# Kernel optimization log

Hardware: AMD Instinct MI355X
Metric: run time of the kernel (lower is better)

Reference implementation:

```python
import jax, jax.numpy as jnp
import numpy as np

# Haar step along H (axis 1 of a (B,H,W) image): average / abs-diff of row pairs.
def _haar_y(img):
    odd, even = img[:, 0::2], img[:, 1::2]
    return (odd + even) / 2.0, jnp.abs(odd - even)

# Haar step along W (axis 2). In the original torch code this is done via
# permute + flip + Y-transform + permute + flip-back; the two flips act on the
# untouched H axis and cancel exactly, so the math reduces to pairing along W.
def _haar_x(img):
    odd, even = img[:, :, 0::2], img[:, :, 1::2]
    return (odd + even) / 2.0, jnp.abs(odd - even)

def _dwt2(img):  # (B,H,W) -> LL, LH, HL, HH each (B,H/2,W/2)
    L, H = _haar_y(img)
    LL, LH = _haar_x(L)
    HL, HH = _haar_x(H)
    return LL, LH, HL, HH

def setup_inputs() -> dict:
    key = jax.random.key(0)
    x = jax.random.uniform(key, (32, 3, 512, 512), dtype=jnp.float32)
    return {"x": x}

def reference(x):
    r, g, b = x[:, 0], x[:, 1], x[:, 2]
    # Level 1
    r1 = _dwt2(r); g1 = _dwt2(g); b1 = _dwt2(b)
    t1 = jnp.stack([*r1, *g1, *b1], axis=1)  # (B,12,H/2,W/2)
    # Level 2 (recursion on LL of each channel)
    r2 = _dwt2(r1[0]); g2 = _dwt2(g1[0]); b2 = _dwt2(b1[0])
    t2 = jnp.stack([*r2, *g2, *b2], axis=1)
    # Level 3
    r3 = _dwt2(r2[0]); g3 = _dwt2(g2[0]); b3 = _dwt2(b2[0])
    t3 = jnp.stack([*r3, *g3, *b3], axis=1)
    # Level 4 -- faithfully reproduces the original bug: the blue-channel
    # level-4 bands are computed from wavelet_L4/H4 left over from the green
    # channel, so b4 == g4.
    r4 = _dwt2(r3[0]); g4 = _dwt2(g3[0]); b4 = g4
    t4 = jnp.stack([*r4, *g4, *b4], axis=1)
    return (t1, t2, t3, t4)
```

## Files before the change

### kernel.cpp

```cpp
#include <hip/hip_runtime.h>

__global__ __launch_bounds__(256) void dwt_level_kernel(
    const float* __restrict__ src, float* __restrict__ dst,
    int W,
    int h, int shift,
    long src_b_stride, long src_c_stride,
    int nC, int dup)
{
    int pid = blockIdx.x * blockDim.x + threadIdx.x;
    int npix = h << shift;
    if (pid >= npix) return;

    int plane = blockIdx.y;
    int b = plane / nC;
    int c = plane - b * nC;

    int jw = pid & ((1 << shift) - 1);
    int i  = pid >> shift;

    const float* sp = src + (long)b * src_b_stride + (long)c * src_c_stride;
    const float4 r0 = *((const float4*)(sp + (long)(2 * i)     * W) + jw);
    const float4 r1 = *((const float4*)(sp + (long)(2 * i + 1) * W) + jw);

    float L00 = (r0.x + r1.x) * 0.5f;
    float L01 = (r0.y + r1.y) * 0.5f;
    float H00 = fabsf(r0.x - r1.x);
    float H01 = fabsf(r0.y - r1.y);
    float L10 = (r0.z + r1.z) * 0.5f;
    float L11 = (r0.w + r1.w) * 0.5f;
    float H10 = fabsf(r0.z - r1.z);
    float H11 = fabsf(r0.w - r1.w);

    float2 ll = make_float2((L00 + L01) * 0.5f, (L10 + L11) * 0.5f);
    float2 lh = make_float2(fabsf(L00 - L01), fabsf(L10 - L11));
    float2 hl = make_float2((H00 + H01) * 0.5f, (H10 + H11) * 0.5f);
    float2 hh = make_float2(fabsf(H00 - H01), fabsf(H10 - H11));

    int w = 2 << shift;
    long hw = (long)h * w;
    float* dp = dst + (long)(b * 12 + 4 * c) * hw + (long)i * w + 2 * jw;

    *(float2*)(dp + 0 * hw) = ll;
    *(float2*)(dp + 1 * hw) = lh;
    *(float2*)(dp + 2 * hw) = hl;
    *(float2*)(dp + 3 * hw) = hh;

    if (dup && c == nC - 1) {
        float* dp2 = dp + 4 * hw;
        *(float2*)(dp2 + 0 * hw) = ll;
        *(float2*)(dp2 + 1 * hw) = lh;
        *(float2*)(dp2 + 2 * hw) = hl;
        *(float2*)(dp2 + 3 * hw) = hh;
    }
}

extern "C" void kernel_launch(void* const* d_in, const int* in_sizes, int n_in,
                              void* d_out, int out_size, void* d_ws, size_t ws_size,
                              hipStream_t stream) {
    const float* x = (const float*)d_in[0];
    float* out = (float*)d_out;

    const long t1_off = 0;
    const long t2_off = t1_off + 32L * 12 * 256 * 256;
    const long t3_off = t2_off + 32L * 12 * 128 * 128;
    const long t4_off = t3_off + 32L * 12 * 64 * 64;

    dim3 blk(256);
    dwt_level_kernel<<<dim3(128, 96), blk, 0, stream>>>(
        x, out + t1_off, 512, 256, 7, 3L * 512 * 512, 512L * 512, 3, 0);
    dwt_level_kernel<<<dim3(32, 96), blk, 0, stream>>>(
        out + t1_off, out + t2_off, 256, 128, 6, 12L * 256 * 256, 4L * 256 * 256, 3, 0);
    dwt_level_kernel<<<dim3(8, 96), blk, 0, stream>>>(
        out + t2_off, out + t3_off, 128, 64, 5, 12L * 128 * 128, 4L * 128 * 128, 3, 0);
    dwt_level_kernel<<<dim3(2, 64), blk, 0, stream>>>(
        out + t3_off, out + t4_off, 64, 32, 4, 12L * 64 * 64, 4L * 64 * 64, 2, 1);
}
```

Measured before the change: 215.7 us.

## Fuse all four Haar DWT levels into one tiled kernel using LDS

Replaces four per-level launches with a single kernel where each block owns a 64x64 input tile per channel plane. It computes level 1 from global memory and keeps each level's LL band in shared memory to compute levels 2-4. This removes the global re-reads of intermediate LL bands and three kernel launches. The cost is more idle threads at the deeper levels, extra block barriers, and narrow per-row stores for the smaller levels.

Result: slower. 223.0 us (+3.4%).

```diff
diff --git a/kernel.cpp b/kernel.cpp
--- a/kernel.cpp
+++ b/kernel.cpp
@@ -1,56 +1,125 @@
 #include <hip/hip_runtime.h>
 
-__global__ __launch_bounds__(256) void dwt_level_kernel(
-    const float* __restrict__ src, float* __restrict__ dst,
-    int W,
-    int h, int shift,
-    long src_b_stride, long src_c_stride,
-    int nC, int dup)
+__global__ __launch_bounds__(256) void dwt_fused_kernel(
+    const float* __restrict__ x, float* __restrict__ out)
 {
-    int pid = blockIdx.x * blockDim.x + threadIdx.x;
-    int npix = h << shift;
-    if (pid >= npix) return;
+    __shared__ float lds1[32 * 36];
+    __shared__ float lds2[16 * 18];
+    __shared__ float lds3[8 * 9];
 
-    int plane = blockIdx.y;
-    int b = plane / nC;
-    int c = plane - b * nC;
+    const int t = threadIdx.x;
+    const int tile = blockIdx.x;
+    const int tx = tile & 7, ty = tile >> 3;
+    const int plane = blockIdx.y;
+    const int b = plane / 3, c = plane - 3 * b;
 
-    int jw = pid & ((1 << shift) - 1);
-    int i  = pid >> shift;
+    const long pbase = (long)(b * 12 + c * 4);
+    const long off2 = 25165824L;
+    const long off3 = 31457280L;
+    const long off4 = 33030144L;
 
-    const float* sp = src + (long)b * src_b_stride + (long)c * src_c_stride;
-    const float4 r0 = *((const float4*)(sp + (long)(2 * i)     * W) + jw);
-    const float4 r1 = *((const float4*)(sp + (long)(2 * i + 1) * W) + jw);
+    {
+        const int oi = t >> 3;
+        const int oj = t & 7;
+        const float* sp = x + (long)(b * 3 + c) * (512 * 512);
+        const int gr = ty * 64 + 2 * oi;
+        const int gc = tx * 64 + 8 * oj;
+        const float4 r0a = *(const float4*)(sp + (long)gr * 512 + gc);
+        const float4 r0b = *(const float4*)(sp + (long)gr * 512 + gc + 4);
+        const float4 r1a = *(const float4*)(sp + (long)(gr + 1) * 512 + gc);
+        const float4 r1b = *(const float4*)(sp + (long)(gr + 1) * 512 + gc + 4);
 
-    float L00 = (r0.x + r1.x) * 0.5f;
-    float L01 = (r0.y + r1.y) * 0.5f;
-    float H00 = fabsf(r0.x - r1.x);
-    float H01 = fabsf(r0.y - r1.y);
-    float L10 = (r0.z + r1.z) * 0.5f;
-    float L11 = (r0.w + r1.w) * 0.5f;
-    float H10 = fabsf(r0.z - r1.z);
-    float H11 = fabsf(r0.w - r1.w);
+        float L0 = (r0a.x + r1a.x) * 0.5f, L1 = (r0a.y + r1a.y) * 0.5f;
+        float H0 = fabsf(r0a.x - r1a.x),   H1 = fabsf(r0a.y - r1a.y);
+        float L2 = (r0a.z + r1a.z) * 0.5f, L3 = (r0a.w + r1a.w) * 0.5f;
+        float H2 = fabsf(r0a.z - r1a.z),   H3 = fabsf(r0a.w - r1a.w);
+        float L4 = (r0b.x + r1b.x) * 0.5f, L5 = (r0b.y + r1b.y) * 0.5f;
+        float H4 = fabsf(r0b.x - r1b.x),   H5 = fabsf(r0b.y - r1b.y);
+        float L6 = (r0b.z + r1b.z) * 0.5f, L7 = (r0b.w + r1b.w) * 0.5f;
+        float H6 = fabsf(r0b.z - r1b.z),   H7 = fabsf(r0b.w - r1b.w);
 
-    float2 ll = make_float2((L00 + L01) * 0.5f, (L10 + L11) * 0.5f);
-    float2 lh = make_float2(fabsf(L00 - L01), fabsf(L10 - L11));
-    float2 hl = make_float2((H00 + H01) * 0.5f, (H10 + H11) * 0.5f);
-    float2 hh = make_float2(fabsf(H00 - H01), fabsf(H10 - H11));
+        float4 ll = make_float4((L0 + L1) * 0.5f, (L2 + L3) * 0.5f,
+                                (L4 + L5) * 0.5f, (L6 + L7) * 0.5f);
+        float4 lh = make_float4(fabsf(L0 - L1), fabsf(L2 - L3),
+                                fabsf(L4 - L5), fabsf(L6 - L7));
+        float4 hl = make_float4((H0 + H1) * 0.5f, (H2 + H3) * 0.5f,
+                                (H4 + H5) * 0.5f, (H6 + H7) * 0.5f);
+        float4 hh = make_float4(fabsf(H0 - H1), fabsf(H2 - H3),
+                                fabsf(H4 - H5), fabsf(H6 - H7));
 
-    int w = 2 << shift;
-    long hw = (long)h * w;
-    float* dp = dst + (long)(b * 12 + 4 * c) * hw + (long)i * w + 2 * jw;
+        float* dp = out + (long)(ty * 32 + oi) * 256 + (tx * 32 + 4 * oj);
+        *(float4*)(dp + (pbase + 0) * 65536) = ll;
+        *(float4*)(dp + (pbase + 1) * 65536) = lh;
+        *(float4*)(dp + (pbase + 2) * 65536) = hl;
+        *(float4*)(dp + (pbase + 3) * 65536) = hh;
 
-    *(float2*)(dp + 0 * hw) = ll;
-    *(float2*)(dp + 1 * hw) = lh;
-    *(float2*)(dp + 2 * hw) = hl;
-    *(float2*)(dp + 3 * hw) = hh;
+        *(float4*)(lds1 + oi * 36 + 4 * oj) = ll;
+    }
+    __syncthreads();
 
-    if (dup && c == nC - 1) {
-        float* dp2 = dp + 4 * hw;
-        *(float2*)(dp2 + 0 * hw) = ll;
-        *(float2*)(dp2 + 1 * hw) = lh;
-        *(float2*)(dp2 + 2 * hw) = hl;
-        *(float2*)(dp2 + 3 * hw) = hh;
+    {
+        const int i2 = t >> 4, j2 = t & 15;
+        float a  = lds1[(2 * i2) * 36 + 2 * j2];
+        float bb = lds1[(2 * i2) * 36 + 2 * j2 + 1];
+        float cc = lds1[(2 * i2 + 1) * 36 + 2 * j2];
+        float dd = lds1[(2 * i2 + 1) * 36 + 2 * j2 + 1];
+        float L0 = (a + cc) * 0.5f, L1 = (bb + dd) * 0.5f;
+        float Ha = fabsf(a - cc),   Hb = fabsf(bb - dd);
+        float ll = (L0 + L1) * 0.5f, lh = fabsf(L0 - L1);
+        float hl = (Ha + Hb) * 0.5f, hh = fabsf(Ha - Hb);
+
+        float* dp = out + off2 + (long)(ty * 16 + i2) * 128 + (tx * 16 + j2);
+        dp[(pbase + 0) * 16384] = ll;
+        dp[(pbase + 1) * 16384] = lh;
+        dp[(pbase + 2) * 16384] = hl;
+        dp[(pbase + 3) * 16384] = hh;
+        lds2[i2 * 18 + j2] = ll;
+    }
+    __syncthreads();
+
+    if (t < 64) {
+        const int i3 = t >> 3, j3 = t & 7;
+        float a  = lds2[(2 * i3) * 18 + 2 * j3];
+        float bb = lds2[(2 * i3) * 18 + 2 * j3 + 1];
+        float cc = lds2[(2 * i3 + 1) * 18 + 2 * j3];
+        float dd = lds2[(2 * i3 + 1) * 18 + 2 * j3 + 1];
+        float L0 = (a + cc) * 0.5f, L1 = (bb + dd) * 0.5f;
+        float Ha = fabsf(a - cc),   Hb = fabsf(bb - dd);
+        float ll = (L0 + L1) * 0.5f, lh = fabsf(L0 - L1);
+        float hl = (Ha + Hb) * 0.5f, hh = fabsf(Ha - Hb);
+
+        float* dp = out + off3 + (long)(ty * 8 + i3) * 64 + (tx * 8 + j3);
+        dp[(pbase + 0) * 4096] = ll;
+        dp[(pbase + 1) * 4096] = lh;
+        dp[(pbase + 2) * 4096] = hl;
+        dp[(pbase + 3) * 4096] = hh;
+        lds3[i3 * 9 + j3] = ll;
+    }
+    __syncthreads();
+
+    if (t < 16 && c < 2) {
+        const int i4 = t >> 2, j4 = t & 3;
+        float a  = lds3[(2 * i4) * 9 + 2 * j4];
+        float bb = lds3[(2 * i4) * 9 + 2 * j4 + 1];
+        float cc = lds3[(2 * i4 + 1) * 9 + 2 * j4];
+        float dd = lds3[(2 * i4 + 1) * 9 + 2 * j4 + 1];
+        float L0 = (a + cc) * 0.5f, L1 = (bb + dd) * 0.5f;
+        float Ha = fabsf(a - cc),   Hb = fabsf(bb - dd);
+        float ll = (L0 + L1) * 0.5f, lh = fabsf(L0 - L1);
+        float hl = (Ha + Hb) * 0.5f, hh = fabsf(Ha - Hb);
+
+        float* dp = out + off4 + (long)(ty * 4 + i4) * 32 + (tx * 4 + j4);
+        dp[(pbase + 0) * 1024] = ll;
+        dp[(pbase + 1) * 1024] = lh;
+        dp[(pbase + 2) * 1024] = hl;
+        dp[(pbase + 3) * 1024] = hh;
+        if (c == 1) {
+            float* dq = dp + 4 * 1024;
+            dq[(pbase + 0) * 1024] = ll;
+            dq[(pbase + 1) * 1024] = lh;
+            dq[(pbase + 2) * 1024] = hl;
+            dq[(pbase + 3) * 1024] = hh;
+        }
     }
 }
 
@@ -59,19 +128,5 @@
                               hipStream_t stream) {
     const float* x = (const float*)d_in[0];
     float* out = (float*)d_out;
-
-    const long t1_off = 0;
-    const long t2_off = t1_off + 32L * 12 * 256 * 256;
-    const long t3_off = t2_off + 32L * 12 * 128 * 128;
-    const long t4_off = t3_off + 32L * 12 * 64 * 64;
-
-    dim3 blk(256);
-    dwt_level_kernel<<<dim3(128, 96), blk, 0, stream>>>(
-        x, out + t1_off, 512, 256, 7, 3L * 512 * 512, 512L * 512, 3, 0);
-    dwt_level_kernel<<<dim3(32, 96), blk, 0, stream>>>(
-        out + t1_off, out + t2_off, 256, 128, 6, 12L * 256 * 256, 4L * 256 * 256, 3, 0);
-    dwt_level_kernel<<<dim3(8, 96), blk, 0, stream>>>(
-        out + t2_off, out + t3_off, 128, 64, 5, 12L * 128 * 128, 4L * 128 * 128, 3, 0);
-    dwt_level_kernel<<<dim3(2, 64), blk, 0, stream>>>(
-        out + t3_off, out + t4_off, 64, 32, 4, 12L * 64 * 64, 4L * 64 * 64, 2, 1);
+    dwt_fused_kernel<<<dim3(64, 96), dim3(256), 0, stream>>>(x, out);
 }
```
